# Optimization experiments

Hardware: AMD Instinct MI355X
Metric: run time of the kernel (lower is better)

## Reference

```python
import jax, jax.numpy as jnp
import numpy as np

N_E = 1024
E_DIM = 64
BETA = 0.25


def setup_inputs() -> dict:
    key = jax.random.key(0)
    k1, k2 = jax.random.split(key)
    z = jax.random.normal(k1, (16, E_DIM, 64, 64), dtype=jnp.float32)
    # embedding initialized uniform(-1/n_e, 1/n_e) as in the torch module
    emb = jax.random.uniform(k2, (N_E, E_DIM), dtype=jnp.float32,
                             minval=-1.0 / N_E, maxval=1.0 / N_E)
    return {"z": z, "emb": emb}


def reference(z, emb):
    n_e, e_dim = emb.shape
    # NCHW -> NHWC, flatten to tokens
    zp = jnp.transpose(z, (0, 2, 3, 1))            # [B,H,W,C]
    zf = zp.reshape(-1, e_dim)                      # [N,C]
    # squared distances ||zf||^2 + ||e||^2 - 2 zf e^T  -> [N, n_e]
    d = (jnp.sum(zf * zf, axis=1, keepdims=True)
         + jnp.sum(emb * emb, axis=1)
         - 2.0 * jnp.matmul(zf, emb.T))
    idx = jnp.argmin(d, axis=1)                     # [N]
    # one-hot @ emb is exactly a gather
    z_q = emb[idx].reshape(zp.shape)                # [B,H,W,C]
    loss = (jnp.mean((jax.lax.stop_gradient(z_q) - zp) ** 2)
            + BETA * jnp.mean((z_q - jax.lax.stop_gradient(zp)) ** 2))
    # straight-through estimator
    z_q = zp + jax.lax.stop_gradient(z_q - zp)
    # perplexity from codeword usage histogram
    counts = jax.ops.segment_sum(jnp.ones_like(idx, dtype=zf.dtype), idx,
                                 num_segments=n_e)
    e_mean = counts / zf.shape[0]
    perplexity = jnp.exp(-jnp.sum(e_mean * jnp.log(e_mean + 1e-10)))
    min_encoding_indices = idx.reshape(z.shape[0], -1).astype(jnp.int32)
    z_q = jnp.transpose(z_q, (0, 3, 1, 2))          # back to NCHW
    return z_q, loss, perplexity, min_encoding_indices
```

## Files before the change

kernel.cpp:

```cpp
#include <hip/hip_runtime.h>

#define TOKS 65536
#define ED 64
#define NE 1024
#define CH_STRIDE 4096
#define B_STRIDE 262144

typedef __bf16 bf16x8 __attribute__((ext_vector_type(8)));
typedef float f32x16 __attribute__((ext_vector_type(16)));
typedef unsigned short ushort_t;
typedef unsigned int uint_t;


__device__ __forceinline__ ushort_t f2bf(float x) {
    uint_t u = __float_as_uint(x);
    uint_t r = u + 0x7FFFu + ((u >> 16) & 1u);
    return (ushort_t)(r >> 16);
}

__global__ __launch_bounds__(256) void vq_prep_e(const float* __restrict__ emb,
                                                 ushort_t* __restrict__ efrag,
                                                 float* __restrict__ enorm,
                                                 int* __restrict__ hist) {
    const int tid = threadIdx.x;
    const int w = tid >> 6, lane = tid & 63;
    const int j = blockIdx.x * 4 + w;

    const float e = emb[j * 64 + lane];
    const float sq = __fmul_rn(e, e);
    float acc = sq;
    acc = __fadd_rn(acc, __shfl_down(sq, 8, 64));
    acc = __fadd_rn(acc, __shfl_down(sq, 16, 64));
    acc = __fadd_rn(acc, __shfl_down(sq, 24, 64));
    acc = __fadd_rn(acc, __shfl_down(sq, 32, 64));
    acc = __fadd_rn(acc, __shfl_down(sq, 40, 64));
    acc = __fadd_rn(acc, __shfl_down(sq, 48, 64));
    acc = __fadd_rn(acc, __shfl_down(sq, 56, 64));
    float x = __fadd_rn(acc, __shfl_down(acc, 1, 64));
    float y = __fadd_rn(x, __shfl_down(x, 2, 64));
    float zn = __fadd_rn(y, __shfl_down(y, 4, 64));
    if (lane == 0) enorm[j] = zn;

    const ushort_t h = f2bf(-2.0f * e);
    const int ct = j >> 5, m = j & 31;
    const int ks = lane >> 4, kh = (lane >> 3) & 1, i = lane & 7;
    efrag[(size_t)((ct * 4 + ks) * 512) + (m + 32 * kh) * 8 + i] = h;

    if (blockIdx.x < 4) hist[blockIdx.x * 256 + tid] = 0;
}

__global__ __launch_bounds__(256, 4) void vq_main(
    const float* __restrict__ z,
    const ushort_t* __restrict__ efrag,
    const float* __restrict__ enorm,
    const float* __restrict__ emb,
    float* __restrict__ zq,
    float* __restrict__ out_idx,
    int* __restrict__ hist,
    double* __restrict__ lossPart) {
    __shared__ float z_s[64][72];
    __shared__ uint_t skey[4][2][32][2][2];
    __shared__ float s_zn[64];
    __shared__ unsigned long long s_res[64];
    __shared__ uint_t s_cand[256];
    __shared__ int s_cnt;
    __shared__ double wsum[4];

    const int tid = threadIdx.x;
    const int w = tid >> 6, lane = tid & 63;
    const int t0 = blockIdx.x * 64;
    const int b = t0 >> 12, hw0 = t0 & 4095;
    const float* zbase = z + (size_t)b * B_STRIDE + hw0;

    {
        const int c = tid >> 2, u0 = (tid & 3) * 16;
        const float* src = zbase + (size_t)c * CH_STRIDE + u0;
        float4 f0 = *(const float4*)(src);
        float4 f1 = *(const float4*)(src + 4);
        float4 f2 = *(const float4*)(src + 8);
        float4 f3 = *(const float4*)(src + 12);
        z_s[u0 +  0][c] = f0.x; z_s[u0 +  1][c] = f0.y;
        z_s[u0 +  2][c] = f0.z; z_s[u0 +  3][c] = f0.w;
        z_s[u0 +  4][c] = f1.x; z_s[u0 +  5][c] = f1.y;
        z_s[u0 +  6][c] = f1.z; z_s[u0 +  7][c] = f1.w;
        z_s[u0 +  8][c] = f2.x; z_s[u0 +  9][c] = f2.y;
        z_s[u0 + 10][c] = f2.z; z_s[u0 + 11][c] = f2.w;
        z_s[u0 + 12][c] = f3.x; z_s[u0 + 13][c] = f3.y;
        z_s[u0 + 14][c] = f3.z; z_s[u0 + 15][c] = f3.w;
    }
    if (tid < 64) s_res[tid] = 0xFFFFFFFFFFFFFFFFull;
    if (tid == 0) s_cnt = 0;
    __syncthreads();

    const int n = lane & 31, kh = lane >> 5;

    bf16x8 zbA[4], zbB[4];
    #pragma unroll
    for (int ks = 0; ks < 4; ++ks) {
        float4 a0 = *(const float4*)&z_s[n][ks * 16 + kh * 8];
        float4 a1 = *(const float4*)&z_s[n][ks * 16 + kh * 8 + 4];
        float4 b0 = *(const float4*)&z_s[32 + n][ks * 16 + kh * 8];
        float4 b1 = *(const float4*)&z_s[32 + n][ks * 16 + kh * 8 + 4];
        const float av[8] = {a0.x, a0.y, a0.z, a0.w, a1.x, a1.y, a1.z, a1.w};
        const float bv[8] = {b0.x, b0.y, b0.z, b0.w, b1.x, b1.y, b1.z, b1.w};
        #pragma unroll
        for (int i = 0; i < 8; ++i) {
            union { ushort_t u; __bf16 bh; } ca, cb;
            ca.u = f2bf(av[i]);
            cb.u = f2bf(bv[i]);
            zbA[ks][i] = ca.bh;
            zbB[ks][i] = cb.bh;
        }
    }

    uint_t kA0 = 0xFFFFFFFFu, kA1 = 0xFFFFFFFFu;
    uint_t kB0 = 0xFFFFFFFFu, kB1 = 0xFFFFFFFFu;
    const bf16x8* eg = (const bf16x8*)efrag;
    const int rot = blockIdx.x & 7;

    int gct = w * 8 + rot;
    bf16x8 ah0 = eg[(size_t)(gct * 4 + 0) * 64 + lane];
    bf16x8 ah1 = eg[(size_t)(gct * 4 + 1) * 64 + lane];
    bf16x8 ah2 = eg[(size_t)(gct * 4 + 2) * 64 + lane];
    bf16x8 ah3 = eg[(size_t)(gct * 4 + 3) * 64 + lane];

    for (int ct = 0; ct < 8; ++ct) {
        const int gnext = w * 8 + ((ct + 1 + rot) & 7);
        bf16x8 nx0, nx1, nx2, nx3;
        if (ct < 7) {
            nx0 = eg[(size_t)(gnext * 4 + 0) * 64 + lane];
            nx1 = eg[(size_t)(gnext * 4 + 1) * 64 + lane];
            nx2 = eg[(size_t)(gnext * 4 + 2) * 64 + lane];
            nx3 = eg[(size_t)(gnext * 4 + 3) * 64 + lane];
        }
        const int jb = gct * 32 + 4 * kh;

        f32x16 accA;
        #pragma unroll
        for (int r = 0; r < 16; ++r) accA[r] = 0.25f;
        accA = __builtin_amdgcn_mfma_f32_32x32x16_bf16(ah0, zbA[0], accA, 0, 0, 0);
        accA = __builtin_amdgcn_mfma_f32_32x32x16_bf16(ah1, zbA[1], accA, 0, 0, 0);
        accA = __builtin_amdgcn_mfma_f32_32x32x16_bf16(ah2, zbA[2], accA, 0, 0, 0);
        accA = __builtin_amdgcn_mfma_f32_32x32x16_bf16(ah3, zbA[3], accA, 0, 0, 0);

        f32x16 accB;
        #pragma unroll
        for (int r = 0; r < 16; ++r) accB[r] = 0.25f;
        accB = __builtin_amdgcn_mfma_f32_32x32x16_bf16(ah0, zbB[0], accB, 0, 0, 0);
        accB = __builtin_amdgcn_mfma_f32_32x32x16_bf16(ah1, zbB[1], accB, 0, 0, 0);
        accB = __builtin_amdgcn_mfma_f32_32x32x16_bf16(ah2, zbB[2], accB, 0, 0, 0);
        accB = __builtin_amdgcn_mfma_f32_32x32x16_bf16(ah3, zbB[3], accB, 0, 0, 0);

        #pragma unroll
        for (int r = 0; r < 16; ++r) {
            const uint_t jbits = (uint_t)(jb + (r & 3) + 8 * (r >> 2));
            uint_t keyA = (__float_as_uint(accA[r]) & 0xFFFFFC00u) | jbits;
            uint_t mxA = max(kA0, keyA);
            kA1 = min(kA1, mxA);
            kA0 = min(kA0, keyA);
            uint_t keyB = (__float_as_uint(accB[r]) & 0xFFFFFC00u) | jbits;
            uint_t mxB = max(kB0, keyB);
            kB1 = min(kB1, mxB);
            kB0 = min(kB0, keyB);
        }
        ah0 = nx0; ah1 = nx1; ah2 = nx2; ah3 = nx3;
        gct = gnext;
    }

    skey[w][0][n][kh][0] = kA0; skey[w][0][n][kh][1] = kA1;
    skey[w][1][n][kh][0] = kB0; skey[w][1][n][kh][1] = kB1;
    __syncthreads();

    const int t_loc = tid >> 2, m = tid & 3;
    const int tile = t_loc >> 5, nn = t_loc & 31;
    {
        uint_t ck[4];
        ck[0] = skey[m][tile][nn][0][0];
        ck[1] = skey[m][tile][nn][0][1];
        ck[2] = skey[m][tile][nn][1][0];
        ck[3] = skey[m][tile][nn][1][1];
        uint_t kmin = min(min(ck[0], ck[1]), min(ck[2], ck[3]));
        kmin = min(kmin, (uint_t)__shfl_xor((int)kmin, 1, 64));
        kmin = min(kmin, (uint_t)__shfl_xor((int)kmin, 2, 64));
        const float thr = __uint_as_float(kmin & 0xFFFFFC00u) + 4.0e-4f;
        #pragma unroll
        for (int s = 0; s < 4; ++s) {
            if (__uint_as_float(ck[s] & 0xFFFFFC00u) <= thr) {
                int pos = atomicAdd(&s_cnt, 1);
                if (pos < 256)
                    s_cand[pos] = ((uint_t)t_loc << 10) | (ck[s] & 1023u);
            }
        }
    }
    {
        float a0 = z_s[t_loc][m];
        float ra = __fmul_rn(a0, a0);
        float b0 = z_s[t_loc][m + 4];
        float rb = __fmul_rn(b0, b0);
        #pragma unroll
        for (int i = 1; i < 8; ++i) {
            float av = z_s[t_loc][m + 8 * i];
            ra = __fadd_rn(ra, __fmul_rn(av, av));
            float bv = z_s[t_loc][m + 4 + 8 * i];
            rb = __fadd_rn(rb, __fmul_rn(bv, bv));
        }
        float xa = __fadd_rn(ra, __shfl_xor(ra, 1, 64));
        float A = __fadd_rn(xa, __shfl_xor(xa, 2, 64));
        float xb = __fadd_rn(rb, __shfl_xor(rb, 1, 64));
        float B = __fadd_rn(xb, __shfl_xor(xb, 2, 64));
        if (m == 0) s_zn[t_loc] = __fadd_rn(A, B);
    }
    __syncthreads();

    {
        const int cnt = s_cnt;
        if (tid < cnt && tid < 256) {
            const uint_t cd = s_cand[tid];
            const int tok = (int)(cd >> 10), j = (int)(cd & 1023u);
            const float* e = emb + (size_t)j * 64;
            float a0 = 0.f;
            #pragma unroll
            for (int k4 = 0; k4 < 16; ++k4) {
                float4 z4 = *(const float4*)&z_s[tok][k4 * 4];
                float4 e4 = *(const float4*)(e + k4 * 4);
                a0 = __fmaf_rn(z4.x, e4.x, a0);
                a0 = __fmaf_rn(z4.y, e4.y, a0);
                a0 = __fmaf_rn(z4.z, e4.z, a0);
                a0 = __fmaf_rn(z4.w, e4.w, a0);
            }
            float d = __fsub_rn(__fadd_rn(s_zn[tok], enorm[j]), 2.0f * a0);
            unsigned long long key =
                ((unsigned long long)__float_as_uint(d) << 10)
                | (unsigned long long)j;
            atomicMin(&s_res[tok], key);
        }
    }
    __syncthreads();

    const int bj = (int)(s_res[t_loc] & 1023u);
    if (m == 0) {
        out_idx[t0 + t_loc] = (float)bj;
        atomicAdd(&hist[bj], 1);
    }
    double ls = 0.0;
    {
        const float* e = emb + (size_t)bj * 64 + m * 16;
        float4 e0 = *(const float4*)(e);
        float4 e1 = *(const float4*)(e + 4);
        float4 e2 = *(const float4*)(e + 8);
        float4 e3 = *(const float4*)(e + 12);
        float4 zv0 = *(const float4*)&z_s[t_loc][m * 16];
        float4 zv1 = *(const float4*)&z_s[t_loc][m * 16 + 4];
        float4 zv2 = *(const float4*)&z_s[t_loc][m * 16 + 8];
        float4 zv3 = *(const float4*)&z_s[t_loc][m * 16 + 12];
        float df;
        df = e0.x - zv0.x; ls += (double)(df * df);
        df = e0.y - zv0.y; ls += (double)(df * df);
        df = e0.z - zv0.z; ls += (double)(df * df);
        df = e0.w - zv0.w; ls += (double)(df * df);
        df = e1.x - zv1.x; ls += (double)(df * df);
        df = e1.y - zv1.y; ls += (double)(df * df);
        df = e1.z - zv1.z; ls += (double)(df * df);
        df = e1.w - zv1.w; ls += (double)(df * df);
        df = e2.x - zv2.x; ls += (double)(df * df);
        df = e2.y - zv2.y; ls += (double)(df * df);
        df = e2.z - zv2.z; ls += (double)(df * df);
        df = e2.w - zv2.w; ls += (double)(df * df);
        df = e3.x - zv3.x; ls += (double)(df * df);
        df = e3.y - zv3.y; ls += (double)(df * df);
        df = e3.z - zv3.z; ls += (double)(df * df);
        df = e3.w - zv3.w; ls += (double)(df * df);
        *(float4*)&z_s[t_loc][m * 16] = e0;
        *(float4*)&z_s[t_loc][m * 16 + 4] = e1;
        *(float4*)&z_s[t_loc][m * 16 + 8] = e2;
        *(float4*)&z_s[t_loc][m * 16 + 12] = e3;
    }
    #pragma unroll
    for (int off = 32; off > 0; off >>= 1) ls += __shfl_down(ls, off, 64);
    if (lane == 0) wsum[w] = ls;
    __syncthreads();
    if (tid == 0)
        lossPart[blockIdx.x] = wsum[0] + wsum[1] + wsum[2] + wsum[3];

    {
        const int c = tid >> 2, u0 = (tid & 3) * 16;
        float4 f0, f1, f2, f3;
        f0.x = z_s[u0 +  0][c]; f0.y = z_s[u0 +  1][c];
        f0.z = z_s[u0 +  2][c]; f0.w = z_s[u0 +  3][c];
        f1.x = z_s[u0 +  4][c]; f1.y = z_s[u0 +  5][c];
        f1.z = z_s[u0 +  6][c]; f1.w = z_s[u0 +  7][c];
        f2.x = z_s[u0 +  8][c]; f2.y = z_s[u0 +  9][c];
        f2.z = z_s[u0 + 10][c]; f2.w = z_s[u0 + 11][c];
        f3.x = z_s[u0 + 12][c]; f3.y = z_s[u0 + 13][c];
        f3.z = z_s[u0 + 14][c]; f3.w = z_s[u0 + 15][c];
        float* dst = zq + (size_t)b * B_STRIDE + (size_t)c * CH_STRIDE + hw0 + u0;
        *(float4*)(dst) = f0;
        *(float4*)(dst + 4) = f1;
        *(float4*)(dst + 8) = f2;
        *(float4*)(dst + 12) = f3;
    }
}

__global__ __launch_bounds__(256) void vq_final(const int* __restrict__ hist,
                                                const double* __restrict__ lossPart,
                                                float* __restrict__ outs) {
    __shared__ double red[256];
    __shared__ double red2[256];
    double acc = 0.0;
    for (int j = threadIdx.x; j < NE; j += 256) {
        double em = (double)hist[j] * (1.0 / 65536.0);
        acc += em * log(em + 1e-10);
    }
    double lsum = 0.0;
    for (int j = threadIdx.x; j < 1024; j += 256) lsum += lossPart[j];
    red[threadIdx.x] = acc;
    red2[threadIdx.x] = lsum;
    __syncthreads();
    for (int s = 128; s > 0; s >>= 1) {
        if (threadIdx.x < s) {
            red[threadIdx.x] += red[threadIdx.x + s];
            red2[threadIdx.x] += red2[threadIdx.x + s];
        }
        __syncthreads();
    }
    if (threadIdx.x == 0) {
        outs[0] = (float)(1.25 * red2[0] * (1.0 / 4194304.0));
        outs[1] = (float)exp(-red[0]);
    }
}

extern "C" void kernel_launch(void* const* d_in, const int* in_sizes, int n_in,
                              void* d_out, int out_size, void* d_ws, size_t ws_size,
                              hipStream_t stream) {
    const float* z = (const float*)d_in[0];
    const float* emb = (const float*)d_in[1];
    float* out = (float*)d_out;

    char* ws = (char*)d_ws;
    ushort_t* efrag = (ushort_t*)ws;
    float* enorm = (float*)(ws + 131072);
    int* hist = (int*)(ws + 135168);
    double* lossPart = (double*)(ws + 143360);

    float* zq = out;
    float* scalars = out + 4194304;
    float* out_idx = out + 4194306;

    vq_prep_e<<<256, 256, 0, stream>>>(emb, efrag, enorm, hist);
    vq_main<<<1024, 256, 0, stream>>>(z, efrag, enorm, emb, zq, out_idx, hist, lossPart);
    vq_final<<<1, 256, 0, stream>>>(hist, lossPart, scalars);
}
```

Before: 46.13 us.

## Split fused VQ kernel into separate codebook scan and exact epilogue kernels

The single fused kernel is split in two. A scan kernel runs one wavefront per 32 tokens, loops over all 1024 codewords with MFMA and keeps the top-3 candidate keys per half-lane, then writes them to workspace. An epilogue kernel reloads z, rescores the candidates exactly in fp32, and does the gather, loss and histogram. This drops the cross-wave shared-memory merge, but it adds a kernel launch, global traffic for the candidates, a second read of z, and strided uncoalesced z loads in the scan kernel.

```diff
diff --git a/kernel.cpp b/kernel.cpp
--- a/kernel.cpp
+++ b/kernel.cpp
@@ -49,9 +49,71 @@
     if (blockIdx.x < 4) hist[blockIdx.x * 256 + tid] = 0;
 }
 
-__global__ __launch_bounds__(256, 4) void vq_main(
+__global__ __launch_bounds__(64) void vq_scan(
     const float* __restrict__ z,
     const ushort_t* __restrict__ efrag,
+    uint_t* __restrict__ cand) {
+    const int lane = threadIdx.x;
+    const int t0 = blockIdx.x * 32;
+    const int b = t0 >> 12, hw0 = t0 & 4095;
+    const float* zbase = z + (size_t)b * B_STRIDE + hw0;
+    const int n = lane & 31, kh = lane >> 5;
+
+    bf16x8 zb[4];
+    #pragma unroll
+    for (int ks = 0; ks < 4; ++ks) {
+        #pragma unroll
+        for (int i = 0; i < 8; ++i) {
+            union { ushort_t u; __bf16 bh; } ca;
+            ca.u = f2bf(zbase[(size_t)(ks * 16 + kh * 8 + i) * CH_STRIDE + n]);
+            zb[ks][i] = ca.bh;
+        }
+    }
+
+    uint_t k0 = 0xFFFFFFFFu, k1 = 0xFFFFFFFFu, k2 = 0xFFFFFFFFu;
+    const bf16x8* eg = (const bf16x8*)efrag;
+
+    bf16x8 ah0 = eg[(size_t)0 * 64 + lane];
+    bf16x8 ah1 = eg[(size_t)1 * 64 + lane];
+    bf16x8 ah2 = eg[(size_t)2 * 64 + lane];
+    bf16x8 ah3 = eg[(size_t)3 * 64 + lane];
+
+    for (int ct = 0; ct < 32; ++ct) {
+        bf16x8 nx0, nx1, nx2, nx3;
+        if (ct < 31) {
+            nx0 = eg[(size_t)((ct + 1) * 4 + 0) * 64 + lane];
+            nx1 = eg[(size_t)((ct + 1) * 4 + 1) * 64 + lane];
+            nx2 = eg[(size_t)((ct + 1) * 4 + 2) * 64 + lane];
+            nx3 = eg[(size_t)((ct + 1) * 4 + 3) * 64 + lane];
+        }
+        f32x16 acc;
+        #pragma unroll
+        for (int r = 0; r < 16; ++r) acc[r] = 0.25f;
+        acc = __builtin_amdgcn_mfma_f32_32x32x16_bf16(ah0, zb[0], acc, 0, 0, 0);
+        acc = __builtin_amdgcn_mfma_f32_32x32x16_bf16(ah1, zb[1], acc, 0, 0, 0);
+        acc = __builtin_amdgcn_mfma_f32_32x32x16_bf16(ah2, zb[2], acc, 0, 0, 0);
+        acc = __builtin_amdgcn_mfma_f32_32x32x16_bf16(ah3, zb[3], acc, 0, 0, 0);
+
+        const int jb = ct * 32 + 4 * kh;
+        #pragma unroll
+        for (int r = 0; r < 16; ++r) {
+            uint_t key = (__float_as_uint(acc[r]) & 0xFFFFFC00u)
+                         | (uint_t)(jb + (r & 3) + 8 * (r >> 2));
+            uint_t mx = max(k0, key);
+            k2 = min(k2, max(k1, mx));
+            k1 = min(k1, mx);
+            k0 = min(k0, key);
+        }
+        if (ct < 31) { ah0 = nx0; ah1 = nx1; ah2 = nx2; ah3 = nx3; }
+    }
+
+    uint_t* cp = cand + (size_t)(t0 + n) * 6 + 3 * kh;
+    cp[0] = k0; cp[1] = k1; cp[2] = k2;
+}
+
+__global__ __launch_bounds__(256, 4) void vq_epilogue(
+    const float* __restrict__ z,
+    const uint_t* __restrict__ cand,
     const float* __restrict__ enorm,
     const float* __restrict__ emb,
     float* __restrict__ zq,
@@ -59,11 +121,8 @@
     int* __restrict__ hist,
     double* __restrict__ lossPart) {
     __shared__ float z_s[64][72];
-    __shared__ uint_t skey[4][2][32][2][2];
     __shared__ float s_zn[64];
     __shared__ unsigned long long s_res[64];
-    __shared__ uint_t s_cand[256];
-    __shared__ int s_cnt;
     __shared__ double wsum[4];
 
     const int tid = threadIdx.x;
@@ -89,109 +148,18 @@
         z_s[u0 + 14][c] = f3.z; z_s[u0 + 15][c] = f3.w;
     }
     if (tid < 64) s_res[tid] = 0xFFFFFFFFFFFFFFFFull;
-    if (tid == 0) s_cnt = 0;
-    __syncthreads();
-
-    const int n = lane & 31, kh = lane >> 5;
-
-    bf16x8 zbA[4], zbB[4];
-    #pragma unroll
-    for (int ks = 0; ks < 4; ++ks) {
-        float4 a0 = *(const float4*)&z_s[n][ks * 16 + kh * 8];
-        float4 a1 = *(const float4*)&z_s[n][ks * 16 + kh * 8 + 4];
-        float4 b0 = *(const float4*)&z_s[32 + n][ks * 16 + kh * 8];
-        float4 b1 = *(const float4*)&z_s[32 + n][ks * 16 + kh * 8 + 4];
-        const float av[8] = {a0.x, a0.y, a0.z, a0.w, a1.x, a1.y, a1.z, a1.w};
-        const float bv[8] = {b0.x, b0.y, b0.z, b0.w, b1.x, b1.y, b1.z, b1.w};
-        #pragma unroll
-        for (int i = 0; i < 8; ++i) {
-            union { ushort_t u; __bf16 bh; } ca, cb;
-            ca.u = f2bf(av[i]);
-            cb.u = f2bf(bv[i]);
-            zbA[ks][i] = ca.bh;
-            zbB[ks][i] = cb.bh;
-        }
-    }
-
-    uint_t kA0 = 0xFFFFFFFFu, kA1 = 0xFFFFFFFFu;
-    uint_t kB0 = 0xFFFFFFFFu, kB1 = 0xFFFFFFFFu;
-    const bf16x8* eg = (const bf16x8*)efrag;
-    const int rot = blockIdx.x & 7;
-
-    int gct = w * 8 + rot;
-    bf16x8 ah0 = eg[(size_t)(gct * 4 + 0) * 64 + lane];
-    bf16x8 ah1 = eg[(size_t)(gct * 4 + 1) * 64 + lane];
-    bf16x8 ah2 = eg[(size_t)(gct * 4 + 2) * 64 + lane];
-    bf16x8 ah3 = eg[(size_t)(gct * 4 + 3) * 64 + lane];
-
-    for (int ct = 0; ct < 8; ++ct) {
-        const int gnext = w * 8 + ((ct + 1 + rot) & 7);
-        bf16x8 nx0, nx1, nx2, nx3;
-        if (ct < 7) {
-            nx0 = eg[(size_t)(gnext * 4 + 0) * 64 + lane];
-            nx1 = eg[(size_t)(gnext * 4 + 1) * 64 + lane];
-            nx2 = eg[(size_t)(gnext * 4 + 2) * 64 + lane];
-            nx3 = eg[(size_t)(gnext * 4 + 3) * 64 + lane];
-        }
-        const int jb = gct * 32 + 4 * kh;
-
-        f32x16 accA;
-        #pragma unroll
-        for (int r = 0; r < 16; ++r) accA[r] = 0.25f;
-        accA = __builtin_amdgcn_mfma_f32_32x32x16_bf16(ah0, zbA[0], accA, 0, 0, 0);
-        accA = __builtin_amdgcn_mfma_f32_32x32x16_bf16(ah1, zbA[1], accA, 0, 0, 0);
-        accA = __builtin_amdgcn_mfma_f32_32x32x16_bf16(ah2, zbA[2], accA, 0, 0, 0);
-        accA = __builtin_amdgcn_mfma_f32_32x32x16_bf16(ah3, zbA[3], accA, 0, 0, 0);
-
-        f32x16 accB;
-        #pragma unroll
-        for (int r = 0; r < 16; ++r) accB[r] = 0.25f;
-        accB = __builtin_amdgcn_mfma_f32_32x32x16_bf16(ah0, zbB[0], accB, 0, 0, 0);
-        accB = __builtin_amdgcn_mfma_f32_32x32x16_bf16(ah1, zbB[1], accB, 0, 0, 0);
-        accB = __builtin_amdgcn_mfma_f32_32x32x16_bf16(ah2, zbB[2], accB, 0, 0, 0);
-        accB = __builtin_amdgcn_mfma_f32_32x32x16_bf16(ah3, zbB[3], accB, 0, 0, 0);
-
-        #pragma unroll
-        for (int r = 0; r < 16; ++r) {
-            const uint_t jbits = (uint_t)(jb + (r & 3) + 8 * (r >> 2));
-            uint_t keyA = (__float_as_uint(accA[r]) & 0xFFFFFC00u) | jbits;
-            uint_t mxA = max(kA0, keyA);
-            kA1 = min(kA1, mxA);
-            kA0 = min(kA0, keyA);
-            uint_t keyB = (__float_as_uint(accB[r]) & 0xFFFFFC00u) | jbits;
-            uint_t mxB = max(kB0, keyB);
-            kB1 = min(kB1, mxB);
-            kB0 = min(kB0, keyB);
-        }
-        ah0 = nx0; ah1 = nx1; ah2 = nx2; ah3 = nx3;
-        gct = gnext;
-    }
-
-    skey[w][0][n][kh][0] = kA0; skey[w][0][n][kh][1] = kA1;
-    skey[w][1][n][kh][0] = kB0; skey[w][1][n][kh][1] = kB1;
-    __syncthreads();
 
     const int t_loc = tid >> 2, m = tid & 3;
-    const int tile = t_loc >> 5, nn = t_loc & 31;
-    {
-        uint_t ck[4];
-        ck[0] = skey[m][tile][nn][0][0];
-        ck[1] = skey[m][tile][nn][0][1];
-        ck[2] = skey[m][tile][nn][1][0];
-        ck[3] = skey[m][tile][nn][1][1];
-        uint_t kmin = min(min(ck[0], ck[1]), min(ck[2], ck[3]));
-        kmin = min(kmin, (uint_t)__shfl_xor((int)kmin, 1, 64));
-        kmin = min(kmin, (uint_t)__shfl_xor((int)kmin, 2, 64));
-        const float thr = __uint_as_float(kmin & 0xFFFFFC00u) + 4.0e-4f;
-        #pragma unroll
-        for (int s = 0; s < 4; ++s) {
-            if (__uint_as_float(ck[s] & 0xFFFFFC00u) <= thr) {
-                int pos = atomicAdd(&s_cnt, 1);
-                if (pos < 256)
-                    s_cand[pos] = ((uint_t)t_loc << 10) | (ck[s] & 1023u);
-            }
-        }
-    }
+
+    uint_t ka = cand[(size_t)(t0 + t_loc) * 6 + m];
+    uint_t kb = (m < 2) ? cand[(size_t)(t0 + t_loc) * 6 + m + 4] : 0xFFFFFFFFu;
+    uint_t kmin = min(ka, kb);
+    kmin = min(kmin, (uint_t)__shfl_xor((int)kmin, 1, 64));
+    kmin = min(kmin, (uint_t)__shfl_xor((int)kmin, 2, 64));
+    const float thr = __uint_as_float(kmin & 0xFFFFFC00u) + 4.0e-4f;
+
+    __syncthreads();
+
     {
         float a0 = z_s[t_loc][m];
         float ra = __fmul_rn(a0, a0);
@@ -212,27 +180,27 @@
     }
     __syncthreads();
 
-    {
-        const int cnt = s_cnt;
-        if (tid < cnt && tid < 256) {
-            const uint_t cd = s_cand[tid];
-            const int tok = (int)(cd >> 10), j = (int)(cd & 1023u);
+    #pragma unroll
+    for (int s = 0; s < 2; ++s) {
+        const uint_t ck = s ? kb : ka;
+        if (__uint_as_float(ck & 0xFFFFFC00u) <= thr) {
+            const int j = (int)(ck & 1023u);
             const float* e = emb + (size_t)j * 64;
             float a0 = 0.f;
             #pragma unroll
             for (int k4 = 0; k4 < 16; ++k4) {
-                float4 z4 = *(const float4*)&z_s[tok][k4 * 4];
+                float4 z4 = *(const float4*)&z_s[t_loc][k4 * 4];
                 float4 e4 = *(const float4*)(e + k4 * 4);
                 a0 = __fmaf_rn(z4.x, e4.x, a0);
                 a0 = __fmaf_rn(z4.y, e4.y, a0);
                 a0 = __fmaf_rn(z4.z, e4.z, a0);
                 a0 = __fmaf_rn(z4.w, e4.w, a0);
             }
-            float d = __fsub_rn(__fadd_rn(s_zn[tok], enorm[j]), 2.0f * a0);
+            float d = __fsub_rn(__fadd_rn(s_zn[t_loc], enorm[j]), 2.0f * a0);
             unsigned long long key =
                 ((unsigned long long)__float_as_uint(d) << 10)
                 | (unsigned long long)j;
-            atomicMin(&s_res[tok], key);
+            atomicMin(&s_res[t_loc], key);
         }
     }
     __syncthreads();
@@ -341,12 +309,15 @@
     float* enorm = (float*)(ws + 131072);
     int* hist = (int*)(ws + 135168);
     double* lossPart = (double*)(ws + 143360);
+    uint_t* cand = (uint_t*)(ws + 151552);
 
     float* zq = out;
     float* scalars = out + 4194304;
     float* out_idx = out + 4194306;
 
     vq_prep_e<<<256, 256, 0, stream>>>(emb, efrag, enorm, hist);
-    vq_main<<<1024, 256, 0, stream>>>(z, efrag, enorm, emb, zq, out_idx, hist, lossPart);
+    vq_scan<<<2048, 64, 0, stream>>>(z, efrag, cand);
+    vq_epilogue<<<1024, 256, 0, stream>>>(z, cand, enorm, emb, zq, out_idx,
+                                          hist, lossPart);
     vq_final<<<1, 256, 0, stream>>>(hist, lossPart, scalars);
 }
```

Result: slower. 63.14 us (+36.9%).
